# Kernel optimization log

Measured on AMD Instinct MI355X. Metric: run time of the kernel, lower is better.

The kernel has to match this reference:

```python
import jax, jax.numpy as jnp
import numpy as np

SEARCH = 7
KNN = 7
SIGMA = 1.0
CUTOFF = 1.0
NCLASSES = 20
H, W, N = 64, 2048, 131072


def _inv_gauss_flat(k, sigma):
    # matches get_gaussian_kernel: 2D gaussian on a k x k grid, normalized, then (1 - g)
    ax = np.arange(k, dtype=np.float32)
    xg = np.tile(ax, (k, 1))          # x varies along columns
    yg = xg.T
    mean = (k - 1) / 2.0
    var = sigma ** 2
    g = np.exp(-((xg - mean) ** 2 + (yg - mean) ** 2) / (2.0 * var)) / (2.0 * np.pi * var)
    g = g / g.sum()
    return (1.0 - g).reshape(-1).astype(np.float32)  # [k*k], row-major like F.unfold

_INV_GAUSS = jnp.asarray(_inv_gauss_flat(SEARCH, SIGMA))


def setup_inputs() -> dict:
    key = jax.random.key(0)
    k1, k2, k3, k4, k5 = jax.random.split(key, 5)
    proj_range = jax.random.normal(k1, (H, W), dtype=jnp.float32)  # negatives exercise the <0 -> inf path
    unproj_range = jax.random.uniform(k2, (N,), dtype=jnp.float32)
    proj_argmax = jax.random.randint(k3, (H, W), 0, NCLASSES)
    px = jax.random.randint(k4, (N,), 0, W)
    py = jax.random.randint(k5, (N,), 0, H)
    return {"proj_range": proj_range, "unproj_range": unproj_range,
            "proj_argmax": proj_argmax, "px": px, "py": py}


def reference(proj_range, unproj_range, proj_argmax, px, py):
    pad = (SEARCH - 1) // 2
    S2 = SEARCH * SEARCH
    # F.unfold flattens the kernel row-major: index i -> (dy, dx) = (i // S, i % S)
    dy = jnp.repeat(jnp.arange(SEARCH) - pad, SEARCH)   # [S2]
    dx = jnp.tile(jnp.arange(SEARCH) - pad, SEARCH)     # [S2]

    rows = py[:, None] + dy[None, :]                    # [N, S2]; zero-padded in H
    cols = (px[:, None] + dx[None, :]) % W              # circular padding in W
    valid = (rows >= 0) & (rows < H)
    rows_c = jnp.clip(rows, 0, H - 1)

    nb_range = jnp.where(valid, proj_range[rows_c, cols], 0.0)        # zero pad like F.unfold
    nb_range = jnp.where(nb_range < 0, jnp.inf, nb_range)
    center = (S2 - 1) // 2
    nb_range = nb_range.at[:, center].set(unproj_range)

    k2d = jnp.abs(nb_range - unproj_range[:, None]) * _INV_GAUSS[None, :]  # [N, S2]
    neg_vals, knn_idx = jax.lax.top_k(-k2d, KNN)        # k smallest distances
    knn_dist = -neg_vals                                # == gather(k2d, knn_idx)

    nb_arg = jnp.where(valid, proj_argmax[rows_c, cols], 0)            # zero pad -> class 0
    knn_arg = jnp.take_along_axis(nb_arg, knn_idx, axis=1)             # [N, KNN]
    if CUTOFF > 0:
        knn_arg = jnp.where(knn_dist > CUTOFF, NCLASSES, knn_arg)

    votes = jax.nn.one_hot(knn_arg, NCLASSES + 1, dtype=proj_range.dtype).sum(axis=1)  # [N, C+1]
    knn_out = jnp.argmax(votes[:, 1:-1], axis=1) + 1    # torch: votes[:, 1:-1].argmax + 1
    return knn_out
```

## Files before the change

kernel.cpp:

```cpp
#include <hip/hip_runtime.h>
#include <math.h>

#define SEARCH 7
#define PAD 3
#define S2 49
#define KNN 7
#define NCLASSES 20
#define H 64
#define W 2048
#define NPTS 131072
#define NTILES 32
#define TROWS 70
#define TCOLS 70
#define SPT 32
#define SLICE (NPTS / SPT)
#define KBLOCK 256
#define QCAP 512

#define SENTINEL_BITS 0x7FE0000000000000ull
#define CUTOFF_KEYMAX 0x4000000FE000003Full

struct InvG { float v[S2]; };

#define INSF(KEY) do {                                                  \
    double _x = (KEY);                                                  \
    double _t;                                                          \
    _t = fmin(s0, _x); _x = fmax(s0, _x); s0 = _t;                      \
    _t = fmin(s1, _x); _x = fmax(s1, _x); s1 = _t;                      \
    _t = fmin(s2, _x); _x = fmax(s2, _x); s2 = _t;                      \
    _t = fmin(s3, _x); _x = fmax(s3, _x); s3 = _t;                      \
    _t = fmin(s4, _x); _x = fmax(s4, _x); s4 = _t;                      \
    _t = fmin(s5, _x); _x = fmax(s5, _x); s5 = _t;                      \
    s6 = fmin(s6, _x);                                                  \
} while (0)

#define CAND(J, RB, DX) do {                                            \
    float nb = ftile[(RB) + (DX)];                                      \
    nb = (nb < 0.0f) ? __builtin_inff() : nb;                           \
    float d = fabsf(nb - u) * invg.v[J];                                \
    unsigned long long kb = (1ull << 62)                                \
        | ((unsigned long long)__float_as_uint(d) << 6)                 \
        | (unsigned)(J);                                                \
    INSF(__longlong_as_double((long long)kb));                          \
} while (0)

__global__ __launch_bounds__(KBLOCK, 4) void knn_kernel(
    const float* __restrict__ proj_range,
    const float* __restrict__ unproj_range,
    const int* __restrict__ proj_argmax,
    const int* __restrict__ pxv,
    const int* __restrict__ pyv,
    int* __restrict__ outv,
    InvG invg)
{
    __shared__ float  ftile[TROWS * TCOLS];
    __shared__ unsigned queue[QCAP];
    __shared__ int qcnt;

    const int tid  = threadIdx.x;
    const int t    = blockIdx.x >> 5;
    const int sub  = blockIdx.x & 31;
    const int tbase = t << 6;
    const int lane = tid & 63;
    const int wave = tid >> 6;

    if (tid == 0) qcnt = 0;

#pragma unroll
    for (int it = 0; it < 18; ++it) {
        int r = it * 4 + wave;
        if (r < TROWS) {
            int sr = r - 3;
            bool vr = (unsigned)sr < (unsigned)H;
            int gb = (vr ? sr : 0) * W;
            int ca = (tbase - 3 + lane) & (W - 1);
            float fv = proj_range[gb + ca];
            ftile[r * TCOLS + lane] = vr ? fv : 0.0f;
            if (lane < TCOLS - 64) {
                int cb = (tbase - 3 + 64 + lane) & (W - 1);
                float fv2 = proj_range[gb + cb];
                ftile[r * TCOLS + 64 + lane] = vr ? fv2 : 0.0f;
            }
        }
    }
    __syncthreads();

    {
        const int4* px4 = (const int4*)pxv;
        int base4 = (sub * SLICE) >> 2;
#pragma unroll
        for (int k = 0; k < 4; ++k) {
            int idx4 = base4 + k * KBLOCK + tid;
            int4 v = px4[idx4];
            int i0x = idx4 * 4;
#pragma unroll
            for (int e = 0; e < 4; ++e) {
                int x = (e == 0) ? v.x : (e == 1) ? v.y : (e == 2) ? v.z : v.w;
                if ((x >> 6) == t) {
                    int i = i0x + e;
                    int y = pyv[i];
                    int pos = atomicAdd(&qcnt, 1);
                    if (pos < QCAP)
                        queue[pos] = (unsigned)i | ((unsigned)(x & 63) << 17)
                                                | ((unsigned)y << 23);
                }
            }
        }
    }
    __syncthreads();
    const int count = min(qcnt, QCAP);

    for (int slot = tid; slot < count; slot += KBLOCK) {
        unsigned pk = queue[slot];
        int i  = (int)(pk & 0x1FFFFu);
        int xl = (int)((pk >> 17) & 63u);
        int y  = (int)((pk >> 23) & 63u);
        float u = unproj_range[i];

        const double sent = __longlong_as_double((long long)SENTINEL_BITS);
        double s0 = sent, s1 = sent, s2 = sent, s3 = sent,
               s4 = sent, s5 = sent, s6 = sent;

        INSF(__longlong_as_double((long long)((1ull << 62) | 24ull)));

#pragma unroll
        for (int dy = -3; dy <= 3; ++dy) {
            int rb = (y + dy + 3) * TCOLS + xl + 3;
#pragma unroll
            for (int dx = -3; dx <= 3; ++dx) {
                const int j = (dy + 3) * 7 + (dx + 3);
                if (j == 24) continue;
                CAND(j, rb, dx);
            }
        }

        const double cutmax = __longlong_as_double((long long)CUTOFF_KEYMAX);
        int c0, c1, c2, c3, c4, c5, c6;
#define CLSK(MK, CK) do {                                                \
        long long kb = __double_as_longlong(MK);                         \
        int j = (int)(kb & 63);                                          \
        bool sel = (MK) <= cutmax;                                       \
        int dy7 = (j * 37) >> 8;                                         \
        int sr = y + dy7 - 3;                                            \
        bool vrow = (unsigned)sr < (unsigned)H;                          \
        int src = min(max(sr, 0), H - 1);                                \
        int colw = (tbase - 3 + xl + (j - dy7 * 7)) & (W - 1);           \
        int cc = proj_argmax[src * W + colw];                            \
        CK = (sel && vrow) ? cc : 0;                                     \
    } while (0)
        CLSK(s0, c0); CLSK(s1, c1); CLSK(s2, c2); CLSK(s3, c3);
        CLSK(s4, c4); CLSK(s5, c5); CLSK(s6, c6);
#undef CLSK

        int n0 = 1, n1 = 1, n2 = 1, n3 = 1, n4 = 1, n5 = 1, n6 = 1;
#define PAIRV(A, B) do { bool e = (c##A == c##B); n##A += e ? 1 : 0; n##B += e ? 1 : 0; } while (0)
        PAIRV(0,1); PAIRV(0,2); PAIRV(0,3); PAIRV(0,4); PAIRV(0,5); PAIRV(0,6);
        PAIRV(1,2); PAIRV(1,3); PAIRV(1,4); PAIRV(1,5); PAIRV(1,6);
        PAIRV(2,3); PAIRV(2,4); PAIRV(2,5); PAIRV(2,6);
        PAIRV(3,4); PAIRV(3,5); PAIRV(3,6);
        PAIRV(4,5); PAIRV(4,6);
        PAIRV(5,6);
#undef PAIRV

        int best = 0;
#define SCORE(K) do {                                                    \
        bool valid = (unsigned)(c##K - 1) < (unsigned)(NCLASSES - 1);    \
        int sc = valid ? ((n##K << 5) | (31 - c##K)) : 0;                \
        best = max(best, sc);                                            \
    } while (0)
        SCORE(0); SCORE(1); SCORE(2); SCORE(3); SCORE(4); SCORE(5); SCORE(6);
#undef SCORE
        int res = (best == 0) ? 1 : (31 - (best & 31));
        __builtin_nontemporal_store(res, &outv[i]);
    }
}

extern "C" void kernel_launch(void* const* d_in, const int* in_sizes, int n_in,
                              void* d_out, int out_size, void* d_ws, size_t ws_size,
                              hipStream_t stream) {
    const float* proj_range   = (const float*)d_in[0];
    const float* unproj_range = (const float*)d_in[1];
    const int*   proj_argmax  = (const int*)d_in[2];
    const int*   px           = (const int*)d_in[3];
    const int*   py           = (const int*)d_in[4];
    int* out = (int*)d_out;

    InvG invg;
    float g[S2];
    for (int yy = 0; yy < SEARCH; ++yy) {
        for (int xx = 0; xx < SEARCH; ++xx) {
            float fdx = (float)xx - 3.0f;
            float fdy = (float)yy - 3.0f;
            float s   = fdx * fdx + fdy * fdy;
            float arg = -s / 2.0f;
            float e   = (float)exp((double)arg);
            float gg  = e / 6.2831855f;
            g[yy * SEARCH + xx] = gg;
        }
    }
    float r[8];
    for (int tt = 0; tt < 8; ++tt) r[tt] = g[tt];
    int ii;
    for (ii = 8; ii + 8 <= 48; ii += 8)
        for (int tt = 0; tt < 8; ++tt) r[tt] += g[ii + tt];
    float ssum = ((r[0] + r[1]) + (r[2] + r[3])) + ((r[4] + r[5]) + (r[6] + r[7]));
    for (; ii < S2; ++ii) ssum += g[ii];
    for (int tt = 0; tt < S2; ++tt) invg.v[tt] = 1.0f - (g[tt] / ssum);

    knn_kernel<<<NTILES * SPT, KBLOCK, 0, stream>>>(
        proj_range, unproj_range, proj_argmax, px, py, out, invg);
}
```

Measured before the change: 19.80 us.

## Split each point's 49-candidate top-k across a lane pair and merge via shuffle

Each query point is now handled by two adjacent lanes. One lane scans candidates 0-23, the other scans 25-48 plus the center. Each keeps a sorted 7-entry list, and the two lists are merged with a bitonic min after xor-shuffles. The per-lane insertion chain is halved so that typical per-tile point counts (about 128) use all 256 threads instead of half of them. The cost is that the class gather and voting work is duplicated in both lanes, plus the added shuffles and per-lane selects of offsets and Gaussian weights.

Measured after the change: 24.96 us. 26.0% more time.

```diff
diff --git a/kernel.cpp b/kernel.cpp
--- a/kernel.cpp
+++ b/kernel.cpp
@@ -34,16 +34,6 @@
     s6 = fmin(s6, _x);                                                  \
 } while (0)
 
-#define CAND(J, RB, DX) do {                                            \
-    float nb = ftile[(RB) + (DX)];                                      \
-    nb = (nb < 0.0f) ? __builtin_inff() : nb;                           \
-    float d = fabsf(nb - u) * invg.v[J];                                \
-    unsigned long long kb = (1ull << 62)                                \
-        | ((unsigned long long)__float_as_uint(d) << 6)                 \
-        | (unsigned)(J);                                                \
-    INSF(__longlong_as_double((long long)kb));                          \
-} while (0)
-
 __global__ __launch_bounds__(KBLOCK, 4) void knn_kernel(
     const float* __restrict__ proj_range,
     const float* __restrict__ unproj_range,
@@ -110,68 +100,100 @@
     __syncthreads();
     const int count = min(qcnt, QCAP);
 
-    for (int slot = tid; slot < count; slot += KBLOCK) {
-        unsigned pk = queue[slot];
-        int i  = (int)(pk & 0x1FFFFu);
-        int xl = (int)((pk >> 17) & 63u);
-        int y  = (int)((pk >> 23) & 63u);
-        float u = unproj_range[i];
-
-        const double sent = __longlong_as_double((long long)SENTINEL_BITS);
-        double s0 = sent, s1 = sent, s2 = sent, s3 = sent,
-               s4 = sent, s5 = sent, s6 = sent;
-
-        INSF(__longlong_as_double((long long)((1ull << 62) | 24ull)));
-
-#pragma unroll
-        for (int dy = -3; dy <= 3; ++dy) {
-            int rb = (y + dy + 3) * TCOLS + xl + 3;
-#pragma unroll
-            for (int dx = -3; dx <= 3; ++dx) {
-                const int j = (dy + 3) * 7 + (dx + 3);
-                if (j == 24) continue;
-                CAND(j, rb, dx);
-            }
-        }
-
-        const double cutmax = __longlong_as_double((long long)CUTOFF_KEYMAX);
-        int c0, c1, c2, c3, c4, c5, c6;
+    const bool isB = (tid & 1) != 0;
+    const int jadd = isB ? 25 : 0;
+
+    for (int base = 0; base < count; base += KBLOCK / 2) {
+        int pt = base + (tid >> 1);
+        if (pt < count) {
+            unsigned pk = queue[pt];
+            int i  = (int)(pk & 0x1FFFFu);
+            int xl = (int)((pk >> 17) & 63u);
+            int y  = (int)((pk >> 23) & 63u);
+            float u = unproj_range[i];
+            int abase = y * TCOLS + xl;
+
+            const double sent = __longlong_as_double((long long)SENTINEL_BITS);
+            double s0 = sent, s1 = sent, s2 = sent, s3 = sent,
+                   s4 = sent, s5 = sent, s6 = sent;
+
+            {
+                unsigned long long ck = isB ? ((1ull << 62) | 24ull) : SENTINEL_BITS;
+                INSF(__longlong_as_double((long long)ck));
+            }
+
+#pragma unroll
+            for (int s = 0; s < 24; ++s) {
+                const int jA = s, jB = s + 25;
+                const int offA = (jA / 7) * TCOLS + (jA % 7);
+                const int offB = (jB / 7) * TCOLS + (jB % 7);
+                int off = isB ? offB : offA;
+                float ig = isB ? invg.v[jB] : invg.v[jA];
+                float nb = ftile[abase + off];
+                nb = (nb < 0.0f) ? __builtin_inff() : nb;
+                float d = fabsf(nb - u) * ig;
+                unsigned long long kb = (1ull << 62)
+                    | ((unsigned long long)__float_as_uint(d) << 6)
+                    | (unsigned)(s + jadd);
+                INSF(__longlong_as_double((long long)kb));
+            }
+
+            double p0 = __shfl_xor(s0, 1, 64);
+            double p1 = __shfl_xor(s1, 1, 64);
+            double p2 = __shfl_xor(s2, 1, 64);
+            double p3 = __shfl_xor(s3, 1, 64);
+            double p4 = __shfl_xor(s4, 1, 64);
+            double p5 = __shfl_xor(s5, 1, 64);
+            double p6 = __shfl_xor(s6, 1, 64);
+            double m0 = fmin(s0, p6);
+            double m1 = fmin(s1, p5);
+            double m2 = fmin(s2, p4);
+            double m3 = fmin(s3, p3);
+            double m4 = fmin(s4, p2);
+            double m5 = fmin(s5, p1);
+            double m6 = fmin(s6, p0);
+
+            const double cutmax = __longlong_as_double((long long)CUTOFF_KEYMAX);
+            int c0, c1, c2, c3, c4, c5, c6;
 #define CLSK(MK, CK) do {                                                \
-        long long kb = __double_as_longlong(MK);                         \
-        int j = (int)(kb & 63);                                          \
-        bool sel = (MK) <= cutmax;                                       \
-        int dy7 = (j * 37) >> 8;                                         \
-        int sr = y + dy7 - 3;                                            \
-        bool vrow = (unsigned)sr < (unsigned)H;                          \
-        int src = min(max(sr, 0), H - 1);                                \
-        int colw = (tbase - 3 + xl + (j - dy7 * 7)) & (W - 1);           \
-        int cc = proj_argmax[src * W + colw];                            \
-        CK = (sel && vrow) ? cc : 0;                                     \
-    } while (0)
-        CLSK(s0, c0); CLSK(s1, c1); CLSK(s2, c2); CLSK(s3, c3);
-        CLSK(s4, c4); CLSK(s5, c5); CLSK(s6, c6);
+            long long kb = __double_as_longlong(MK);                     \
+            int j = (int)(kb & 63);                                      \
+            bool sel = (MK) <= cutmax;                                   \
+            int dy7 = (j * 37) >> 8;                                     \
+            int sr = y + dy7 - 3;                                        \
+            bool vrow = (unsigned)sr < (unsigned)H;                      \
+            int src = min(max(sr, 0), H - 1);                            \
+            int colw = (tbase - 3 + xl + (j - dy7 * 7)) & (W - 1);       \
+            int cc = proj_argmax[src * W + colw];                        \
+            CK = (sel && vrow) ? cc : 0;                                 \
+        } while (0)
+            CLSK(m0, c0); CLSK(m1, c1); CLSK(m2, c2); CLSK(m3, c3);
+            CLSK(m4, c4); CLSK(m5, c5); CLSK(m6, c6);
 #undef CLSK
 
-        int n0 = 1, n1 = 1, n2 = 1, n3 = 1, n4 = 1, n5 = 1, n6 = 1;
+            int n0 = 1, n1 = 1, n2 = 1, n3 = 1, n4 = 1, n5 = 1, n6 = 1;
 #define PAIRV(A, B) do { bool e = (c##A == c##B); n##A += e ? 1 : 0; n##B += e ? 1 : 0; } while (0)
-        PAIRV(0,1); PAIRV(0,2); PAIRV(0,3); PAIRV(0,4); PAIRV(0,5); PAIRV(0,6);
-        PAIRV(1,2); PAIRV(1,3); PAIRV(1,4); PAIRV(1,5); PAIRV(1,6);
-        PAIRV(2,3); PAIRV(2,4); PAIRV(2,5); PAIRV(2,6);
-        PAIRV(3,4); PAIRV(3,5); PAIRV(3,6);
-        PAIRV(4,5); PAIRV(4,6);
-        PAIRV(5,6);
+            PAIRV(0,1); PAIRV(0,2); PAIRV(0,3); PAIRV(0,4); PAIRV(0,5); PAIRV(0,6);
+            PAIRV(1,2); PAIRV(1,3); PAIRV(1,4); PAIRV(1,5); PAIRV(1,6);
+            PAIRV(2,3); PAIRV(2,4); PAIRV(2,5); PAIRV(2,6);
+            PAIRV(3,4); PAIRV(3,5); PAIRV(3,6);
+            PAIRV(4,5); PAIRV(4,6);
+            PAIRV(5,6);
 #undef PAIRV
 
-        int best = 0;
+            int best = 0;
 #define SCORE(K) do {                                                    \
-        bool valid = (unsigned)(c##K - 1) < (unsigned)(NCLASSES - 1);    \
-        int sc = valid ? ((n##K << 5) | (31 - c##K)) : 0;                \
-        best = max(best, sc);                                            \
-    } while (0)
-        SCORE(0); SCORE(1); SCORE(2); SCORE(3); SCORE(4); SCORE(5); SCORE(6);
+            bool valid = (unsigned)(c##K - 1) < (unsigned)(NCLASSES - 1);\
+            int sc = valid ? ((n##K << 5) | (31 - c##K)) : 0;            \
+            best = max(best, sc);                                        \
+        } while (0)
+            SCORE(0); SCORE(1); SCORE(2); SCORE(3); SCORE(4); SCORE(5); SCORE(6);
 #undef SCORE
-        int res = (best == 0) ? 1 : (31 - (best & 31));
-        __builtin_nontemporal_store(res, &outv[i]);
+            if (!isB) {
+                int res = (best == 0) ? 1 : (31 - (best & 31));
+                __builtin_nontemporal_store(res, &outv[i]);
+            }
+        }
     }
 }
 
```
